# Performance work log

Measured on AMD Instinct MI355X. Metric: run time of the kernel, lower is better.

## Reference

```python
import jax, jax.numpy as jnp
import numpy as np

CH = 64
GROUPS = 32
EPS = 1e-5


def setup_inputs() -> dict:
    key = jax.random.key(0)
    ks = jax.random.split(key, 10)
    b, c, h, w = 4, CH, 64, 64
    x = jax.random.normal(ks[0], (b, c, h, w), dtype=jnp.float32)
    s = 1.0 / np.sqrt(c)
    Wq = jax.random.normal(ks[1], (c, c), dtype=jnp.float32) * s
    bq = jnp.zeros((c,), dtype=jnp.float32)
    Wk = jax.random.normal(ks[2], (c, c), dtype=jnp.float32) * s
    bk = jnp.zeros((c,), dtype=jnp.float32)
    Wv = jax.random.normal(ks[3], (c, c), dtype=jnp.float32) * s
    bv = jnp.zeros((c,), dtype=jnp.float32)
    Wo = jax.random.normal(ks[4], (c, c), dtype=jnp.float32) * s
    bo = jnp.zeros((c,), dtype=jnp.float32)
    gamma = jnp.ones((c,), dtype=jnp.float32)
    beta = jnp.zeros((c,), dtype=jnp.float32)
    return {"x": x, "Wq": Wq, "bq": bq, "Wk": Wk, "bk": bk,
            "Wv": Wv, "bv": bv, "Wo": Wo, "bo": bo,
            "gamma": gamma, "beta": beta}


def group_norm(x, gamma, beta):
    b, c, h, w = x.shape
    xg = x.reshape(b, GROUPS, c // GROUPS, h, w)
    mean = jnp.mean(xg, axis=(2, 3, 4), keepdims=True)
    var = jnp.var(xg, axis=(2, 3, 4), keepdims=True)
    xn = ((xg - mean) * jax.lax.rsqrt(var + EPS)).reshape(b, c, h, w)
    return xn * gamma[None, :, None, None] + beta[None, :, None, None]


def conv1x1(x, W, bias):
    # 1x1 conv == channel matmul: x [b,c,h,w], W [out,in]
    return jnp.einsum('bchw,oc->bohw', x, W) + bias[None, :, None, None]


def reference(x, Wq, bq, Wk, bk, Wv, bv, Wo, bo, gamma, beta):
    b, c, h, w = x.shape
    n = h * w
    xn = group_norm(x, gamma, beta)
    q = conv1x1(xn, Wq, bq).reshape(b, c, n)  # [b,c,n]
    k = conv1x1(xn, Wk, bk).reshape(b, c, n)
    v = conv1x1(xn, Wv, bv).reshape(b, c, n)
    scale = 1.0 / jnp.sqrt(jnp.asarray(c, dtype=x.dtype))
    # scores: q^T k -> [b, n_q, n_k]
    attn = jax.nn.softmax(jnp.einsum('bci,bcj->bij', q, k) * scale, axis=-1)
    # out = v @ attn^T -> [b, c, n_q]
    out = jnp.einsum('bcj,bij->bci', v, attn).reshape(b, c, h, w)
    return x + conv1x1(out, Wo, bo)
```

## Files before the change

kernel.cpp:

```cpp
#include <hip/hip_runtime.h>
#include <hip/hip_bf16.h>

#define NPOS 4096
#define KS 72
#define QSCALE 0.18033688011112042f

typedef __attribute__((ext_vector_type(4))) float f32x4;
typedef __attribute__((ext_vector_type(8))) short bf16x8;
typedef __attribute__((ext_vector_type(2))) int i32x2;

__device__ __forceinline__ short f2bf(float f) {
  union { __hip_bfloat16 h; short s; } u;
  u.h = __float2bfloat16(f);
  return u.s;
}
__device__ __forceinline__ int pack_bf16(float lo, float hi) {
  unsigned a = (unsigned short)f2bf(lo);
  unsigned b = (unsigned short)f2bf(hi);
  return (int)(a | (b << 16));
}
__device__ __forceinline__ bf16x8 cvt8(const float* p) {
  f32x4 u = *(const f32x4*)p;
  f32x4 v = *(const f32x4*)(p + 4);
  bf16x8 r;
  r[0] = f2bf(u.x); r[1] = f2bf(u.y); r[2] = f2bf(u.z); r[3] = f2bf(u.w);
  r[4] = f2bf(v.x); r[5] = f2bf(v.y); r[6] = f2bf(v.z); r[7] = f2bf(v.w);
  return r;
}
__device__ __forceinline__ float exp2_hw(float x) { return __builtin_amdgcn_exp2f(x); }

typedef const __attribute__((address_space(1))) void* gas_ptr;
typedef __attribute__((address_space(3))) void* las_ptr;
__device__ __forceinline__ void gload_lds16(const void* g, void* l) {
  __builtin_amdgcn_global_load_lds((gas_ptr)g, (las_ptr)l, 16, 0, 0);
}

__global__ __launch_bounds__(256) void stats_kernel(const float* __restrict__ x,
                                                    float* __restrict__ stats) {
  const int bg = blockIdx.x;
  const f32x4* base = (const f32x4*)(x + (size_t)bg * 8192);
  float s = 0.f, ss = 0.f;
  for (int i = threadIdx.x; i < 2048; i += 256) {
    f32x4 v = base[i];
    s  += v.x + v.y + v.z + v.w;
    ss += v.x * v.x + v.y * v.y + v.z * v.z + v.w * v.w;
  }
  for (int off = 32; off; off >>= 1) {
    s  += __shfl_down(s, off, 64);
    ss += __shfl_down(ss, off, 64);
  }
  __shared__ float red[8];
  const int wave = threadIdx.x >> 6, lane = threadIdx.x & 63;
  if (lane == 0) { red[wave] = s; red[4 + wave] = ss; }
  __syncthreads();
  if (threadIdx.x == 0) {
    float S  = red[0] + red[1] + red[2] + red[3];
    float SS = red[4] + red[5] + red[6] + red[7];
    float mean = S * (1.f / 8192.f);
    float var  = SS * (1.f / 8192.f) - mean * mean;
    stats[2 * bg]     = mean;
    stats[2 * bg + 1] = rsqrtf(var + 1e-5f);
  }
}

__global__ __launch_bounds__(256) void qkv_kernel(
    const float* __restrict__ x,
    const float* __restrict__ Wq, const float* __restrict__ bq,
    const float* __restrict__ Wk, const float* __restrict__ bk,
    const float* __restrict__ Wv, const float* __restrict__ bv,
    const float* __restrict__ gamma, const float* __restrict__ beta,
    const float* __restrict__ stats,
    short* __restrict__ qT, short* __restrict__ kT, short* __restrict__ vC) {
  __shared__ short xn_lds[32 * KS];
  __shared__ short out_lds[32 * 200];

  const int tid  = threadIdx.x;
  const int b    = blockIdx.x >> 7;
  const int pt   = blockIdx.x & 127;
  const int p0   = pt << 5;
  const int wave = tid >> 6;
  const int lane = tid & 63;
  const int quad = lane >> 4;
  const int l16  = lane & 15;

  bf16x8 a_lo[3], a_hi[3];
  float bias_r[3][4];
  {
    const float* Wsrc[3] = {Wq, Wk, Wv};
    const float* Bsrc[3] = {bq, bk, bv};
#pragma unroll
    for (int t = 0; t < 3; t++) {
      const float* wr = Wsrc[t] + (size_t)(wave * 16 + l16) * 64;
      a_lo[t] = cvt8(wr + quad * 8);
      a_hi[t] = cvt8(wr + 32 + quad * 8);
#pragma unroll
      for (int r = 0; r < 4; r++) bias_r[t][r] = Bsrc[t][wave * 16 + quad * 4 + r];
    }
  }

  {
    const int ch = tid >> 2, pg = tid & 3;
    float mean = stats[b * 64 + 2 * (ch >> 1)];
    float rstd = stats[b * 64 + 2 * (ch >> 1) + 1];
    float sc = rstd * gamma[ch];
    float sh = beta[ch] - mean * sc;
    const float* src = x + ((size_t)(b * 64 + ch)) * NPOS + p0 + pg * 8;
    f32x4 v0 = *(const f32x4*)src;
    f32x4 v1 = *(const f32x4*)(src + 4);
    short* d = xn_lds + ch;
    d[(pg * 8 + 0) * KS] = f2bf(fmaf(v0.x, sc, sh));
    d[(pg * 8 + 1) * KS] = f2bf(fmaf(v0.y, sc, sh));
    d[(pg * 8 + 2) * KS] = f2bf(fmaf(v0.z, sc, sh));
    d[(pg * 8 + 3) * KS] = f2bf(fmaf(v0.w, sc, sh));
    d[(pg * 8 + 4) * KS] = f2bf(fmaf(v1.x, sc, sh));
    d[(pg * 8 + 5) * KS] = f2bf(fmaf(v1.y, sc, sh));
    d[(pg * 8 + 6) * KS] = f2bf(fmaf(v1.z, sc, sh));
    d[(pg * 8 + 7) * KS] = f2bf(fmaf(v1.w, sc, sh));
  }
  __syncthreads();

  const f32x4 zero4 = {0.f, 0.f, 0.f, 0.f};
#pragma unroll
  for (int n = 0; n < 2; n++) {
    const short* xr = xn_lds + (n * 16 + l16) * KS;
    bf16x8 b_lo = *(const bf16x8*)(xr + quad * 8);
    bf16x8 b_hi = *(const bf16x8*)(xr + 32 + quad * 8);
#pragma unroll
    for (int t = 0; t < 3; t++) {
      f32x4 c = zero4;
      c = __builtin_amdgcn_mfma_f32_16x16x32_bf16(a_lo[t], b_lo, c, 0, 0, 0);
      c = __builtin_amdgcn_mfma_f32_16x16x32_bf16(a_hi[t], b_hi, c, 0, 0, 0);
      float o0 = c[0] + bias_r[t][0], o1 = c[1] + bias_r[t][1];
      float o2 = c[2] + bias_r[t][2], o3 = c[3] + bias_r[t][3];
      if (t == 0) { o0 *= QSCALE; o1 *= QSCALE; o2 *= QSCALE; o3 *= QSCALE; }
      i32x2 val;
      val.x = pack_bf16(o0, o1);
      val.y = pack_bf16(o2, o3);
      *(i32x2*)(out_lds + (n * 16 + l16) * 200 + t * 64 + wave * 16 + quad * 4) = val;
    }
  }
  __syncthreads();

  {
    const int p = tid >> 3, c8 = (tid & 7) << 3;
    short* qd = qT + ((size_t)(b * NPOS + p0 + p)) * 64 + c8;
    *(bf16x8*)qd = *(const bf16x8*)(out_lds + p * 200 + c8);
    short* kd = kT + ((size_t)(b * NPOS + p0 + p)) * 64 + c8;
    *(bf16x8*)kd = *(const bf16x8*)(out_lds + p * 200 + 64 + c8);
  }
  {
    const int ch = tid >> 2, pg = tid & 3;
    bf16x8 v;
#pragma unroll
    for (int i = 0; i < 8; i++) v[i] = out_lds[(pg * 8 + i) * 200 + 128 + ch];
    *(bf16x8*)(vC + ((size_t)(b * 64 + ch)) * NPOS + p0 + pg * 8) = v;
  }
}

__global__ __launch_bounds__(256) void flash5_kernel(
    const short* __restrict__ qT, const short* __restrict__ kT,
    const short* __restrict__ vC, float* __restrict__ part,
    float* __restrict__ lsum) {
  __shared__ short Kbuf[2][64 * 64];
  __shared__ short Vbuf[2][64 * 64];
  __shared__ short P_lds[4][16 * 64];

  const int raw = blockIdx.x;
  const int bid = ((raw & 7) << 7) + (raw >> 3);
  const int qt    = bid & 63;
  const int chunk = (bid >> 6) & 3;
  const int b     = bid >> 8;
  const int tid   = threadIdx.x;
  const int wave  = tid >> 6;
  const int lane  = tid & 63;
  const int quad  = lane >> 4;
  const int l16   = lane & 15;
  const int r7    = l16 & 7;
  const int m0    = (qt << 6) + (wave << 4);
  const int jbase = chunk << 10;

  const short* qp = qT + ((size_t)(b * NPOS + m0 + l16)) * 64 + quad * 8;
  bf16x8 bq0 = *(const bf16x8*)qp;
  bf16x8 bq1 = *(const bf16x8*)(qp + 32);

  const f32x4 zero4 = {0.f, 0.f, 0.f, 0.f};
  f32x4 o_acc[4] = {zero4, zero4, zero4, zero4};
  float lacc = 0.f;
  short* pw = &P_lds[wave][0];

  auto stage = [&](int bb, int kt2) {
    const int j0s = jbase + (kt2 << 6);
#pragma unroll
    for (int k = 0; k < 2; k++) {
      const int u   = k * 256 + (wave << 6) + lane;
      const int row = u >> 3;
      const int ss  = (u & 7) ^ (row & 7);
      const short* gk = kT + ((size_t)(b * NPOS + j0s + row)) * 64 + ss * 8;
      gload_lds16(gk, &Kbuf[bb][(k * 256 + (wave << 6)) * 8]);
      const short* gv = vC + ((size_t)(b * 64 + row)) * NPOS + j0s + ss * 8;
      gload_lds16(gv, &Vbuf[bb][(k * 256 + (wave << 6)) * 8]);
    }
  };

  stage(0, 0);
  int cur = 0;

#pragma unroll 2
  for (int kt = 0; kt < 16; kt++) {
    if (kt < 15) {
      stage(cur ^ 1, kt + 1);
      asm volatile("s_waitcnt vmcnt(4)" ::: "memory");
    } else {
      asm volatile("s_waitcnt vmcnt(0)" ::: "memory");
    }
    __builtin_amdgcn_sched_barrier(0);
    __builtin_amdgcn_s_barrier();
    __builtin_amdgcn_sched_barrier(0);

    short* prow = pw + l16 * 64;
#pragma unroll
    for (int t = 0; t < 4; t++) {
      const short* kr = &Kbuf[cur][(t * 16 + l16) * 64];
      bf16x8 ka0 = *(const bf16x8*)(kr + ((quad ^ r7) << 3));
      bf16x8 ka1 = *(const bf16x8*)(kr + (((quad + 4) ^ r7) << 3));
      f32x4 acc = zero4;
      acc = __builtin_amdgcn_mfma_f32_16x16x32_bf16(ka0, bq0, acc, 0, 0, 0);
      acc = __builtin_amdgcn_mfma_f32_16x16x32_bf16(ka1, bq1, acc, 0, 0, 0);
      float p0 = exp2_hw(acc[0]), p1 = exp2_hw(acc[1]);
      float p2 = exp2_hw(acc[2]), p3 = exp2_hw(acc[3]);
      lacc += (p0 + p1) + (p2 + p3);
      i32x2 val;
      val.x = pack_bf16(p0, p1);
      val.y = pack_bf16(p2, p3);
      *(i32x2*)(prow + ((t * 16 + quad * 4) ^ (r7 << 3))) = val;
    }

    bf16x8 pb0 = *(const bf16x8*)(prow + ((quad * 8) ^ (r7 << 3)));
    bf16x8 pb1 = *(const bf16x8*)(prow + ((32 + quad * 8) ^ (r7 << 3)));

#pragma unroll
    for (int t = 0; t < 4; t++) {
      const short* vr = &Vbuf[cur][(t * 16 + l16) * 64];
      bf16x8 va0 = *(const bf16x8*)(vr + ((quad ^ r7) << 3));
      bf16x8 va1 = *(const bf16x8*)(vr + (((quad + 4) ^ r7) << 3));
      o_acc[t] = __builtin_amdgcn_mfma_f32_16x16x32_bf16(va0, pb0, o_acc[t], 0, 0, 0);
      o_acc[t] = __builtin_amdgcn_mfma_f32_16x16x32_bf16(va1, pb1, o_acc[t], 0, 0, 0);
    }

    asm volatile("s_waitcnt lgkmcnt(0)" ::: "memory");
    __builtin_amdgcn_sched_barrier(0);
    __builtin_amdgcn_s_barrier();
    cur ^= 1;
  }

  lacc += __shfl_xor(lacc, 16, 64);
  lacc += __shfl_xor(lacc, 32, 64);
  float* base = part + ((size_t)((b * 4 + chunk) * 64 + qt)) * 4096;
  const int col = (wave << 4) + l16;
#pragma unroll
  for (int t = 0; t < 4; t++)
#pragma unroll
    for (int r = 0; r < 4; r++)
      base[(t * 16 + quad * 4 + r) * 64 + col] = o_acc[t][r];
  if (quad == 0) lsum[((size_t)(b * 4 + chunk) << 12) + m0 + l16] = lacc;
}

__global__ __launch_bounds__(256) void co_kernel(
    const float* __restrict__ part, const float* __restrict__ lsum,
    const float* __restrict__ Wo, const float* __restrict__ bo,
    const float* __restrict__ x, float* __restrict__ y) {
  __shared__ float inv[32];
  __shared__ short attn_lds[32 * KS];
  __shared__ float y_lds[64 * 36];

  const int tid   = threadIdx.x;
  const int b     = blockIdx.x >> 7;
  const int pt    = blockIdx.x & 127;
  const int qt    = pt >> 1;
  const int rhalf = (pt & 1) << 5;
  const int p0    = pt << 5;
  const int wave  = tid >> 6;
  const int lane  = tid & 63;
  const int quad  = lane >> 4;
  const int l16   = lane & 15;

  const float* wr = Wo + (size_t)(wave * 16 + l16) * 64;
  bf16x8 a_lo = cvt8(wr + quad * 8);
  bf16x8 a_hi = cvt8(wr + 32 + quad * 8);

  if (tid < 32) {
    float lt = 0.f;
#pragma unroll
    for (int c = 0; c < 4; c++) lt += lsum[((size_t)(b * 4 + c) << 12) + p0 + tid];
    inv[tid] = 1.f / lt;
  }
  __syncthreads();

  {
    const int ch = tid >> 2, g = tid & 3;
    float acc[8];
#pragma unroll
    for (int i = 0; i < 8; i++) acc[i] = 0.f;
#pragma unroll
    for (int c = 0; c < 4; c++) {
      const f32x4* src = (const f32x4*)(part +
          ((size_t)((b * 4 + c) * 64 + qt)) * 4096 + (size_t)ch * 64 + rhalf + g * 8);
      f32x4 v0 = src[0], v1 = src[1];
      acc[0] += v0.x; acc[1] += v0.y; acc[2] += v0.z; acc[3] += v0.w;
      acc[4] += v1.x; acc[5] += v1.y; acc[6] += v1.z; acc[7] += v1.w;
    }
    const float* iv = &inv[g * 8];
#pragma unroll
    for (int i = 0; i < 8; i++) attn_lds[(g * 8 + i) * KS + ch] = f2bf(acc[i] * iv[i]);
  }
  __syncthreads();

  const f32x4 zero4 = {0.f, 0.f, 0.f, 0.f};
#pragma unroll
  for (int n = 0; n < 2; n++) {
    const short* ar = attn_lds + (n * 16 + l16) * KS;
    bf16x8 b_lo = *(const bf16x8*)(ar + quad * 8);
    bf16x8 b_hi = *(const bf16x8*)(ar + 32 + quad * 8);
    f32x4 c = zero4;
    c = __builtin_amdgcn_mfma_f32_16x16x32_bf16(a_lo, b_lo, c, 0, 0, 0);
    c = __builtin_amdgcn_mfma_f32_16x16x32_bf16(a_hi, b_hi, c, 0, 0, 0);
#pragma unroll
    for (int r = 0; r < 4; r++)
      y_lds[(wave * 16 + quad * 4 + r) * 36 + n * 16 + l16] = c[r];
  }
  __syncthreads();

  {
    const int ch = tid >> 2, pg = tid & 3;
    const size_t off = ((size_t)(b * 64 + ch)) * NPOS + p0 + pg * 8;
    const float* xs = x + off;
    float* dst = y + off;
    float bb = bo[ch];
    const float* ys = y_lds + ch * 36 + pg * 8;
    f32x4 x0 = *(const f32x4*)xs, x1 = *(const f32x4*)(xs + 4);
    f32x4 y0 = *(const f32x4*)ys, y1 = *(const f32x4*)(ys + 4);
    f32x4 o0 = {x0.x + bb + y0.x, x0.y + bb + y0.y, x0.z + bb + y0.z, x0.w + bb + y0.w};
    f32x4 o1 = {x1.x + bb + y1.x, x1.y + bb + y1.y, x1.z + bb + y1.z, x1.w + bb + y1.w};
    *(f32x4*)dst = o0;
    *(f32x4*)(dst + 4) = o1;
  }
}

extern "C" void kernel_launch(void* const* d_in, const int* in_sizes, int n_in,
                              void* d_out, int out_size, void* d_ws, size_t ws_size,
                              hipStream_t stream) {
  const float* x     = (const float*)d_in[0];
  const float* Wq    = (const float*)d_in[1];
  const float* bq    = (const float*)d_in[2];
  const float* Wk    = (const float*)d_in[3];
  const float* bk    = (const float*)d_in[4];
  const float* Wv    = (const float*)d_in[5];
  const float* bv    = (const float*)d_in[6];
  const float* Wo    = (const float*)d_in[7];
  const float* bo    = (const float*)d_in[8];
  const float* gamma = (const float*)d_in[9];
  const float* beta  = (const float*)d_in[10];
  float* y = (float*)d_out;

  char* ws = (char*)d_ws;
  float* stats = (float*)ws;
  short* qT   = (short*)(ws + 1024);
  short* kT   = (short*)(ws + 1024 + (1u << 21));
  short* vC   = (short*)(ws + 1024 + (2u << 21));
  float* part = (float*)(ws + 1024 + (3u << 21));
  float* lsum = (float*)(ws + 1024 + (11u << 21));

  stats_kernel<<<dim3(128), dim3(256), 0, stream>>>(x, stats);
  qkv_kernel<<<dim3(512), dim3(256), 0, stream>>>(x, Wq, bq, Wk, bk, Wv, bv,
                                                  gamma, beta, stats, qT, kT, vC);
  flash5_kernel<<<dim3(1024), dim3(256), 0, stream>>>(qT, kT, vC, part, lsum);
  co_kernel<<<dim3(512), dim3(256), 0, stream>>>(part, lsum, Wo, bo, x, y);
}
```

Measured before the change: 123.2 us.

## Switch flash kernel to 32x32 MFMA with register P via permlane32 swap

Rewrites the attention kernel to use 32x32x16 bf16 MFMA tiles, with each wave owning 32 query rows. The probability matrix is moved between MFMA layouts in registers using permlane32_swap instead of a round trip through shared memory. The key range is split into 8 chunks of 512 instead of 4 of 1024, which doubles the partial-output buffer and the reduction work in co_kernel. The partial layout becomes position-major, and co_kernel's reads are adjusted to match. The aim is fewer LDS writes and reads and better MFMA efficiency per instruction, at the cost of more registers, more partial traffic and a launch bound that requests 4 blocks.

```diff
diff --git a/kernel.cpp b/kernel.cpp
--- a/kernel.cpp
+++ b/kernel.cpp
@@ -6,8 +6,10 @@
 #define QSCALE 0.18033688011112042f
 
 typedef __attribute__((ext_vector_type(4))) float f32x4;
+typedef __attribute__((ext_vector_type(16))) float f32x16;
 typedef __attribute__((ext_vector_type(8))) short bf16x8;
 typedef __attribute__((ext_vector_type(2))) int i32x2;
+typedef __attribute__((ext_vector_type(2))) int iv2;
 
 __device__ __forceinline__ short f2bf(float f) {
   union { __hip_bfloat16 h; short s; } u;
@@ -157,36 +159,37 @@
   }
 }
 
-__global__ __launch_bounds__(256) void flash5_kernel(
+__global__ __launch_bounds__(256, 4) void flash6_kernel(
     const short* __restrict__ qT, const short* __restrict__ kT,
     const short* __restrict__ vC, float* __restrict__ part,
     float* __restrict__ lsum) {
   __shared__ short Kbuf[2][64 * 64];
   __shared__ short Vbuf[2][64 * 64];
-  __shared__ short P_lds[4][16 * 64];
 
   const int raw = blockIdx.x;
   const int bid = ((raw & 7) << 7) + (raw >> 3);
-  const int qt    = bid & 63;
-  const int chunk = (bid >> 6) & 3;
+  const int qt    = bid & 31;
+  const int chunk = (bid >> 5) & 7;
   const int b     = bid >> 8;
   const int tid   = threadIdx.x;
   const int wave  = tid >> 6;
   const int lane  = tid & 63;
-  const int quad  = lane >> 4;
-  const int l16   = lane & 15;
-  const int r7    = l16 & 7;
-  const int m0    = (qt << 6) + (wave << 4);
-  const int jbase = chunk << 10;
-
-  const short* qp = qT + ((size_t)(b * NPOS + m0 + l16)) * 64 + quad * 8;
-  bf16x8 bq0 = *(const bf16x8*)qp;
-  bf16x8 bq1 = *(const bf16x8*)(qp + 32);
-
-  const f32x4 zero4 = {0.f, 0.f, 0.f, 0.f};
-  f32x4 o_acc[4] = {zero4, zero4, zero4, zero4};
+  const int hi    = lane >> 5;
+  const int l32   = lane & 31;
+  const int m0w   = (qt << 7) + (wave << 5);
+  const int jbase = chunk << 9;
+
+  bf16x8 bq[4];
+  {
+    const short* qp = qT + ((size_t)(b * NPOS + m0w + l32)) * 64 + hi * 8;
+#pragma unroll
+    for (int cs = 0; cs < 4; cs++) bq[cs] = *(const bf16x8*)(qp + cs * 16);
+  }
+
+  f32x16 oa0, oa1;
+#pragma unroll
+  for (int r = 0; r < 16; r++) { oa0[r] = 0.f; oa1[r] = 0.f; }
   float lacc = 0.f;
-  short* pw = &P_lds[wave][0];
 
   auto stage = [&](int bb, int kt2) {
     const int j0s = jbase + (kt2 << 6);
@@ -206,8 +209,8 @@
   int cur = 0;
 
 #pragma unroll 2
-  for (int kt = 0; kt < 16; kt++) {
-    if (kt < 15) {
+  for (int kt = 0; kt < 8; kt++) {
+    if (kt < 7) {
       stage(cur ^ 1, kt + 1);
       asm volatile("s_waitcnt vmcnt(4)" ::: "memory");
     } else {
@@ -217,34 +220,47 @@
     __builtin_amdgcn_s_barrier();
     __builtin_amdgcn_sched_barrier(0);
 
-    short* prow = pw + l16 * 64;
-#pragma unroll
-    for (int t = 0; t < 4; t++) {
-      const short* kr = &Kbuf[cur][(t * 16 + l16) * 64];
-      bf16x8 ka0 = *(const bf16x8*)(kr + ((quad ^ r7) << 3));
-      bf16x8 ka1 = *(const bf16x8*)(kr + (((quad + 4) ^ r7) << 3));
-      f32x4 acc = zero4;
-      acc = __builtin_amdgcn_mfma_f32_16x16x32_bf16(ka0, bq0, acc, 0, 0, 0);
-      acc = __builtin_amdgcn_mfma_f32_16x16x32_bf16(ka1, bq1, acc, 0, 0, 0);
-      float p0 = exp2_hw(acc[0]), p1 = exp2_hw(acc[1]);
-      float p2 = exp2_hw(acc[2]), p3 = exp2_hw(acc[3]);
-      lacc += (p0 + p1) + (p2 + p3);
-      i32x2 val;
-      val.x = pack_bf16(p0, p1);
-      val.y = pack_bf16(p2, p3);
-      *(i32x2*)(prow + ((t * 16 + quad * 4) ^ (r7 << 3))) = val;
-    }
-
-    bf16x8 pb0 = *(const bf16x8*)(prow + ((quad * 8) ^ (r7 << 3)));
-    bf16x8 pb1 = *(const bf16x8*)(prow + ((32 + quad * 8) ^ (r7 << 3)));
-
-#pragma unroll
-    for (int t = 0; t < 4; t++) {
-      const short* vr = &Vbuf[cur][(t * 16 + l16) * 64];
-      bf16x8 va0 = *(const bf16x8*)(vr + ((quad ^ r7) << 3));
-      bf16x8 va1 = *(const bf16x8*)(vr + (((quad + 4) ^ r7) << 3));
-      o_acc[t] = __builtin_amdgcn_mfma_f32_16x16x32_bf16(va0, pb0, o_acc[t], 0, 0, 0);
-      o_acc[t] = __builtin_amdgcn_mfma_f32_16x16x32_bf16(va1, pb1, o_acc[t], 0, 0, 0);
+#pragma unroll
+    for (int jt = 0; jt < 2; jt++) {
+      f32x16 s;
+#pragma unroll
+      for (int r = 0; r < 16; r++) s[r] = 0.f;
+      const int krow = (jt << 5) + l32;
+      const short* kr = &Kbuf[cur][krow * 64];
+#pragma unroll
+      for (int cs = 0; cs < 4; cs++) {
+        bf16x8 ka = *(const bf16x8*)(kr + (((cs << 1) + hi) ^ (krow & 7)) * 8);
+        s = __builtin_amdgcn_mfma_f32_32x32x16_bf16(ka, bq[cs], s, 0, 0, 0);
+      }
+
+      float p[16];
+#pragma unroll
+      for (int r = 0; r < 16; r++) { p[r] = exp2_hw(s[r]); lacc += p[r]; }
+
+#pragma unroll
+      for (int ks = 0; ks < 2; ks++) {
+        int a0 = pack_bf16(p[ks * 8 + 0], p[ks * 8 + 1]);
+        int b0 = pack_bf16(p[ks * 8 + 4], p[ks * 8 + 5]);
+        int a1 = pack_bf16(p[ks * 8 + 2], p[ks * 8 + 3]);
+        int b1 = pack_bf16(p[ks * 8 + 6], p[ks * 8 + 7]);
+        iv2 r02 = __builtin_amdgcn_permlane32_swap(a0, b0, false, false);
+        iv2 r13 = __builtin_amdgcn_permlane32_swap(a1, b1, false, false);
+        union { bf16x8 v; int w[4]; } pu;
+        pu.w[0] = r02[0]; pu.w[1] = r13[0]; pu.w[2] = r02[1]; pu.w[3] = r13[1];
+        const bf16x8 pa = pu.v;
+
+        const int vs = (jt << 2) + (ks << 1) + hi;
+        {
+          const int vrow = l32;
+          bf16x8 vb = *(const bf16x8*)(&Vbuf[cur][vrow * 64] + ((vs ^ (vrow & 7)) << 3));
+          oa0 = __builtin_amdgcn_mfma_f32_32x32x16_bf16(pa, vb, oa0, 0, 0, 0);
+        }
+        {
+          const int vrow = 32 + l32;
+          bf16x8 vb = *(const bf16x8*)(&Vbuf[cur][vrow * 64] + ((vs ^ (vrow & 7)) << 3));
+          oa1 = __builtin_amdgcn_mfma_f32_32x32x16_bf16(pa, vb, oa1, 0, 0, 0);
+        }
+      }
     }
 
     asm volatile("s_waitcnt lgkmcnt(0)" ::: "memory");
@@ -253,16 +269,15 @@
     cur ^= 1;
   }
 
-  lacc += __shfl_xor(lacc, 16, 64);
   lacc += __shfl_xor(lacc, 32, 64);
-  float* base = part + ((size_t)((b * 4 + chunk) * 64 + qt)) * 4096;
-  const int col = (wave << 4) + l16;
-#pragma unroll
-  for (int t = 0; t < 4; t++)
-#pragma unroll
-    for (int r = 0; r < 4; r++)
-      base[(t * 16 + quad * 4 + r) * 64 + col] = o_acc[t][r];
-  if (quad == 0) lsum[((size_t)(b * 4 + chunk) << 12) + m0 + l16] = lacc;
+  float* pb = part + ((size_t)(b * 8 + chunk) << 18);
+#pragma unroll
+  for (int r = 0; r < 16; r++) {
+    const int m = m0w + (r & 3) + ((r >> 2) << 3) + (hi << 2);
+    pb[(size_t)m * 64 + l32]      = oa0[r];
+    pb[(size_t)m * 64 + 32 + l32] = oa1[r];
+  }
+  if (lane < 32) lsum[((size_t)(b * 8 + chunk) << 12) + m0w + l32] = lacc;
 }
 
 __global__ __launch_bounds__(256) void co_kernel(
@@ -276,8 +291,6 @@
   const int tid   = threadIdx.x;
   const int b     = blockIdx.x >> 7;
   const int pt    = blockIdx.x & 127;
-  const int qt    = pt >> 1;
-  const int rhalf = (pt & 1) << 5;
   const int p0    = pt << 5;
   const int wave  = tid >> 6;
   const int lane  = tid & 63;
@@ -291,27 +304,27 @@
   if (tid < 32) {
     float lt = 0.f;
 #pragma unroll
-    for (int c = 0; c < 4; c++) lt += lsum[((size_t)(b * 4 + c) << 12) + p0 + tid];
+    for (int c = 0; c < 8; c++) lt += lsum[((size_t)(b * 8 + c) << 12) + p0 + tid];
     inv[tid] = 1.f / lt;
   }
   __syncthreads();
 
   {
-    const int ch = tid >> 2, g = tid & 3;
+    const int r = tid >> 3, c8 = (tid & 7) << 3;
     float acc[8];
 #pragma unroll
     for (int i = 0; i < 8; i++) acc[i] = 0.f;
 #pragma unroll
-    for (int c = 0; c < 4; c++) {
-      const f32x4* src = (const f32x4*)(part +
-          ((size_t)((b * 4 + c) * 64 + qt)) * 4096 + (size_t)ch * 64 + rhalf + g * 8);
+    for (int c = 0; c < 8; c++) {
+      const f32x4* src = (const f32x4*)(part + ((size_t)(b * 8 + c) << 18) +
+                                        (size_t)(p0 + r) * 64 + c8);
       f32x4 v0 = src[0], v1 = src[1];
       acc[0] += v0.x; acc[1] += v0.y; acc[2] += v0.z; acc[3] += v0.w;
       acc[4] += v1.x; acc[5] += v1.y; acc[6] += v1.z; acc[7] += v1.w;
     }
-    const float* iv = &inv[g * 8];
-#pragma unroll
-    for (int i = 0; i < 8; i++) attn_lds[(g * 8 + i) * KS + ch] = f2bf(acc[i] * iv[i]);
+    const float iv = inv[r];
+#pragma unroll
+    for (int i = 0; i < 8; i++) attn_lds[r * KS + c8 + i] = f2bf(acc[i] * iv);
   }
   __syncthreads();
 
@@ -368,11 +381,11 @@
   short* kT   = (short*)(ws + 1024 + (1u << 21));
   short* vC   = (short*)(ws + 1024 + (2u << 21));
   float* part = (float*)(ws + 1024 + (3u << 21));
-  float* lsum = (float*)(ws + 1024 + (11u << 21));
+  float* lsum = (float*)(ws + 1024 + (19u << 21));
 
   stats_kernel<<<dim3(128), dim3(256), 0, stream>>>(x, stats);
   qkv_kernel<<<dim3(512), dim3(256), 0, stream>>>(x, Wq, bq, Wk, bk, Wv, bv,
                                                   gamma, beta, stats, qT, kT, vC);
-  flash5_kernel<<<dim3(1024), dim3(256), 0, stream>>>(qT, kT, vC, part, lsum);
+  flash6_kernel<<<dim3(1024), dim3(256), 0, stream>>>(qT, kT, vC, part, lsum);
   co_kernel<<<dim3(512), dim3(256), 0, stream>>>(part, lsum, Wo, bo, x, y);
 }
```

Result: faster. 119.1 us (-3.3%).
